# Optimization experiments

Measured on AMD Instinct MI355X. Metric: run time of the kernel, lower is better.

The kernel has to match this reference:

```python
import jax, jax.numpy as jnp
import numpy as np

H = 16          # num_heads
D_NOPE = 128    # qk_nope_head_dim
D_ROPE = 64     # qk_rope_head_dim
D_QK = 192      # qk_head_dim
D_V = 128       # v_head_dim
THETA = 10000.0
EPS = 1e-6


def rmsnorm(x, w):
    x32 = x.astype(jnp.float32)
    x32 = x32 * jax.lax.rsqrt(jnp.mean(x32 * x32, axis=-1, keepdims=True) + EPS)
    return (x32 * w).astype(x.dtype)


def rope_cos_sin(seq_len, dim, dtype):
    inv_freq = 1.0 / (THETA ** (jnp.arange(0, dim, 2, dtype=jnp.float32) / dim))  # [dim/2]
    t = jnp.arange(seq_len, dtype=jnp.float32)
    freqs = jnp.outer(t, inv_freq)  # [T, dim/2]
    return jnp.cos(freqs).astype(dtype), jnp.sin(freqs).astype(dtype)


def apply_rope(x, cos, sin):
    # x: [B, T, h, D_ROPE]; GPT-NeoX style half-split rotation
    d2 = x.shape[-1] // 2
    x1, x2 = x[..., :d2], x[..., d2:]
    c = cos[None, :, None, :]
    s = sin[None, :, None, :]
    return jnp.concatenate([x1 * c - x2 * s, x2 * c + x1 * s], axis=-1)


def setup_inputs() -> dict:
    key = jax.random.key(0)
    ks = jax.random.split(key, 8)
    B, T, D = 2, 2048, 2048
    q_lora, kv_lora = 1536, 512
    def w(k, fan_in, fan_out):
        return jax.random.normal(k, (fan_in, fan_out), dtype=jnp.float32) * (1.0 / np.sqrt(fan_in))
    return {
        "hidden_states": jax.random.normal(ks[0], (B, T, D), dtype=jnp.float32),
        "Wq_a": w(ks[1], D, q_lora),
        "q_norm_w": jnp.ones((q_lora,), dtype=jnp.float32),
        "Wq_b": w(ks[2], q_lora, H * D_QK),
        "Wk_rope": w(ks[3], D, D_ROPE),
        "Wkv_a": w(ks[4], D, kv_lora),
        "kv_norm_w": jnp.ones((kv_lora,), dtype=jnp.float32),
        "Wkv_b": w(ks[5], kv_lora, H * (D_NOPE + D_V)),
        "Wo": w(ks[6], H * D_V, D),
    }


def reference(hidden_states, Wq_a, q_norm_w, Wq_b, Wk_rope, Wkv_a, kv_norm_w, Wkv_b, Wo):
    B, T, D = hidden_states.shape
    # Q: LoRA down -> RMSNorm -> up, split into nope/rope parts
    q = rmsnorm(hidden_states @ Wq_a, q_norm_w) @ Wq_b          # [B,T,H*D_QK]
    q = q.reshape(B, T, H, D_QK)
    q_pass, q_rot = q[..., :D_NOPE], q[..., D_NOPE:]
    # KV: LoRA down -> RMSNorm -> up, split into k_nope / v
    kv = rmsnorm(hidden_states @ Wkv_a, kv_norm_w) @ Wkv_b      # [B,T,H*(D_NOPE+D_V)]
    kv = kv.reshape(B, T, H, D_NOPE + D_V)
    k_pass, v = kv[..., :D_NOPE], kv[..., D_NOPE:]
    # decoupled rope key (shared across heads)
    k_rot = (hidden_states @ Wk_rope)[:, :, None, :]            # [B,T,1,D_ROPE]
    cos, sin = rope_cos_sin(T, D_ROPE, hidden_states.dtype)
    q_rot = apply_rope(q_rot, cos, sin)
    k_rot = apply_rope(k_rot, cos, sin)
    k_rot = jnp.broadcast_to(k_rot, (B, T, H, D_ROPE))
    qf = jnp.concatenate([q_pass, q_rot], axis=-1)              # [B,T,H,D_QK]
    kf = jnp.concatenate([k_pass, k_rot], axis=-1)              # [B,T,H,D_QK]
    # causal attention, flash_attn default scale = D_QK ** -0.5
    scale = 1.0 / np.sqrt(D_QK)
    scores = jnp.einsum("bqhd,bkhd->bhqk", qf, kf) * scale
    mask = jnp.tril(jnp.ones((T, T), dtype=bool))
    scores = jnp.where(mask[None, None], scores, jnp.finfo(scores.dtype).min)
    p = jax.nn.softmax(scores, axis=-1)
    o = jnp.einsum("bhqk,bkhd->bqhd", p, v)                     # [B,T,H,D_V]
    o = o.reshape(B, T, H * D_V) @ Wo
    return o
```

## Files before the change

### kernel.cpp

```cpp
#include <hip/hip_runtime.h>
#include <cstdint>
#include <cstddef>

typedef unsigned short u16;
typedef __bf16 bf16x8 __attribute__((ext_vector_type(8)));
typedef float f32x4 __attribute__((ext_vector_type(4)));
typedef short short8 __attribute__((ext_vector_type(8)));

#define DEVI static __device__ __forceinline__

DEVI u16 f2bf(float f) {
    unsigned u = __builtin_bit_cast(unsigned, f);
    u += 0x7fffu + ((u >> 16) & 1u);
    return (u16)(u >> 16);
}
DEVI float bf2f(u16 h) {
    unsigned u = ((unsigned)h) << 16;
    return __builtin_bit_cast(float, u);
}

namespace cfg {
constexpr int B = 2, T = 2048, BT = 4096, D = 2048, QL = 1536, KVL = 512, H = 16;
constexpr int DQK = 192, DROPE = 64, DV = 128, HD = H * DQK, KVD = H * 256;
constexpr int NCAT = 2176;
}

__global__ void cvt_bf16_k(const float* __restrict__ in, u16* __restrict__ out, int n4) {
    for (int i = blockIdx.x * blockDim.x + threadIdx.x; i < n4; i += gridDim.x * blockDim.x) {
        float4 v = reinterpret_cast<const float4*>(in)[i];
        ushort4 o;
        o.x = f2bf(v.x); o.y = f2bf(v.y); o.z = f2bf(v.z); o.w = f2bf(v.w);
        reinterpret_cast<ushort4*>(out)[i] = o;
    }
}

__global__ void transpose_cvt_k(const float* __restrict__ in, u16* __restrict__ out, int R, int C) {
    __shared__ float tile[32][33];
    int tx = threadIdx.x & 31, ty = threadIdx.x >> 5;
    int c0 = blockIdx.x * 32, r0 = blockIdx.y * 32;
#pragma unroll
    for (int j = 0; j < 4; ++j)
        tile[ty + j * 8][tx] = in[(size_t)(r0 + ty + j * 8) * C + c0 + tx];
    __syncthreads();
#pragma unroll
    for (int j = 0; j < 4; ++j)
        out[(size_t)(c0 + ty + j * 8) * R + r0 + tx] = f2bf(tile[tx][ty + j * 8]);
}

__global__ void rmsnorm_k(const u16* __restrict__ x, const float* __restrict__ w,
                          u16* __restrict__ y, int C, int xs) {
    int row = blockIdx.x, tid = threadIdx.x;
    const u16* xr = x + (size_t)row * xs;
    u16* yr = y + (size_t)row * C;
    float ss = 0.f;
    for (int i = tid; i < C; i += 256) { float v = bf2f(xr[i]); ss += v * v; }
#pragma unroll
    for (int m = 32; m >= 1; m >>= 1) ss += __shfl_xor(ss, m);
    __shared__ float red[4];
    if ((tid & 63) == 0) red[tid >> 6] = ss;
    __syncthreads();
    float tot = red[0] + red[1] + red[2] + red[3];
    float rs = rsqrtf(tot / C + 1e-6f);
    for (int i = tid; i < C; i += 256) yr[i] = f2bf(bf2f(xr[i]) * rs * w[i]);
}

__global__ void rope_tab_k(float* __restrict__ ct, float* __restrict__ st) {
    int idx = blockIdx.x * 256 + threadIdx.x;
    int t = idx >> 5, i = idx & 31;
    float inv = powf(10000.f, -(float)i / 32.f);
    float f = (float)t * inv;
    ct[idx] = cosf(f);
    st[idx] = sinf(f);
}

__global__ void rope_apply_k(u16* __restrict__ x, const float* __restrict__ ct,
                             const float* __restrict__ st, int nrows, int rstride,
                             int roff, int rows_per_t) {
    int idx = blockIdx.x * 256 + threadIdx.x;
    if (idx >= nrows * 32) return;
    int row = idx >> 5, i = idx & 31;
    int t = (row / rows_per_t) % cfg::T;
    u16* p = x + (size_t)row * rstride + roff;
    float x1 = bf2f(p[i]), x2 = bf2f(p[32 + i]);
    float c = ct[t * 32 + i], s = st[t * 32 + i];
    p[i] = f2bf(x1 * c - x2 * s);
    p[32 + i] = f2bf(x2 * c + x1 * s);
}

__global__ __launch_bounds__(256) void vtrans_k(const u16* __restrict__ kv,
                                                u16* __restrict__ vt) {
    using namespace cfg;
    __shared__ u16 tl[64][136];
    const int bh = blockIdx.x, t0 = blockIdx.y * 64;
    const int b = bh >> 4, h = bh & 15;
    const int tid = threadIdx.x;
#pragma unroll
    for (int it = 0; it < 4; ++it) {
        int id = tid + it * 256, r = id >> 4, c8 = id & 15;
        short8 v = *reinterpret_cast<const short8*>(
            kv + ((size_t)(b * T + t0 + r) * H + h) * 256 + 128 + c8 * 8);
        *reinterpret_cast<short8*>(&tl[r][c8 * 8]) = v;
    }
    __syncthreads();
#pragma unroll
    for (int it = 0; it < 4; ++it) {
        int id = tid + it * 256, d = id >> 3, tc = id & 7;
        short8 v;
#pragma unroll
        for (int j = 0; j < 8; ++j) v[j] = (short)tl[tc * 8 + j][d];
        *reinterpret_cast<short8*>(vt + ((size_t)bh * 128 + d) * T + t0 + tc * 8) = v;
    }
}

template <int BM, int BN, int BK, int WM, int WN, bool OUTF32>
__global__ __launch_bounds__((BM / WM) * (BN / WN) * 64) void gemm_bt_k(
    const u16* __restrict__ A, const u16* __restrict__ Bt, void* __restrict__ Cv,
    int M, int N, int K, float cscale) {
    constexpr int NW = (BM / WM) * (BN / WN);
    constexpr int MFR = WM / 16, NFR = WN / 16;
    constexpr int NWN = BN / WN;
    __shared__ u16 As[BM * BK];
    __shared__ u16 Bs[BN * BK];
    const int tid = threadIdx.x, lane = tid & 63, wid = tid >> 6;
    const int wr = wid / NWN, wc = wid % NWN;
    const int tM = blockIdx.x * BM, tN = blockIdx.y * BN;
    const int lr = lane & 15, hi = lane >> 4;
    f32x4 acc[MFR][NFR] = {};
    for (int k0 = 0; k0 < K; k0 += BK) {
        constexpr int ACH = BM * BK * 2 / NW;
#pragma unroll
        for (int c = 0; c < ACH / 1024; ++c) {
            int loff = wid * ACH + c * 1024;
            int eidx = (loff >> 1) + lane * 8;
            const u16* src = A + (size_t)(tM + eidx / BK) * K + k0 + (eidx % BK);
            __builtin_amdgcn_global_load_lds(
                (const __attribute__((address_space(1))) void*)src,
                (__attribute__((address_space(3))) void*)((char*)As + loff), 16, 0, 0);
        }
        constexpr int BCH = BN * BK * 2 / NW;
#pragma unroll
        for (int c = 0; c < BCH / 1024; ++c) {
            int loff = wid * BCH + c * 1024;
            int eidx = (loff >> 1) + lane * 8;
            const u16* src = Bt + (size_t)(tN + eidx / BK) * K + k0 + (eidx % BK);
            __builtin_amdgcn_global_load_lds(
                (const __attribute__((address_space(1))) void*)src,
                (__attribute__((address_space(3))) void*)((char*)Bs + loff), 16, 0, 0);
        }
        __syncthreads();
#pragma unroll
        for (int kk = 0; kk < BK / 32; ++kk) {
            bf16x8 af[MFR], bfv[NFR];
#pragma unroll
            for (int mi = 0; mi < MFR; ++mi)
                af[mi] = *reinterpret_cast<const bf16x8*>(&As[(wr * WM + mi * 16 + lr) * BK + kk * 32 + hi * 8]);
#pragma unroll
            for (int ni = 0; ni < NFR; ++ni)
                bfv[ni] = *reinterpret_cast<const bf16x8*>(&Bs[(wc * WN + ni * 16 + lr) * BK + kk * 32 + hi * 8]);
#pragma unroll
            for (int mi = 0; mi < MFR; ++mi)
#pragma unroll
                for (int ni = 0; ni < NFR; ++ni)
                    acc[mi][ni] = __builtin_amdgcn_mfma_f32_16x16x32_bf16(af[mi], bfv[ni], acc[mi][ni], 0, 0, 0);
        }
        __syncthreads();
    }
#pragma unroll
    for (int mi = 0; mi < MFR; ++mi)
#pragma unroll
        for (int ni = 0; ni < NFR; ++ni)
#pragma unroll
            for (int r = 0; r < 4; ++r) {
                int row = tM + wr * WM + mi * 16 + hi * 4 + r;
                int col = tN + wc * WN + ni * 16 + lr;
                float v = acc[mi][ni][r] * cscale;
                if (OUTF32)
                    ((float*)Cv)[(size_t)row * N + col] = v;
                else
                    ((u16*)Cv)[(size_t)row * N + col] = f2bf(v);
            }
}

namespace acfg {
constexpr int QB = 64, KB = 64, KS = 200, VTS = 72, PS = 72;
constexpr int NQT = cfg::T / QB;
}
__global__ __launch_bounds__(256) void mla_attn_k(const u16* __restrict__ q,
                                                  const u16* __restrict__ kv,
                                                  const u16* __restrict__ kr, int krs,
                                                  const u16* __restrict__ vtg,
                                                  u16* __restrict__ o) {
    using namespace cfg;
    using namespace acfg;
    __shared__ u16 Ks[KB * KS];
    __shared__ u16 Vt[DV * VTS];
    __shared__ u16 Pl[4 * 16 * PS];
    const int bid = blockIdx.x;
    const int bh = bid & 31;
    const int qt = NQT - 1 - (bid >> 5);
    const int b = bh >> 4, h = bh & 15;
    const int q0 = qt * QB;
    const int tid = threadIdx.x, lane = tid & 63, w = tid >> 6;
    const int lr = lane & 15, hi = lane >> 4;

    bf16x8 qf[6];
    {
        int row = q0 + w * 16 + lr;
        const u16* qp = q + ((size_t)(b * T + row) * H + h) * DQK;
#pragma unroll
        for (int ks = 0; ks < 6; ++ks)
            qf[ks] = *reinterpret_cast<const bf16x8*>(qp + ks * 32 + hi * 8);
    }
    f32x4 oacc[8] = {};
    float lsum[4] = {0.f, 0.f, 0.f, 0.f};

    const int nkb = qt + 1;
#pragma unroll 1
    for (int kb = 0; kb < nkb; ++kb) {
        const int kt0 = kb * KB;
#pragma unroll
        for (int it = 0; it < 4; ++it) {
            int id = tid + it * 256, r = id >> 4, c8 = id & 15;
            short8 v = *reinterpret_cast<const short8*>(
                kv + ((size_t)(b * T + kt0 + r) * H + h) * 256 + c8 * 8);
            *reinterpret_cast<short8*>(&Ks[r * KS + c8 * 8]) = v;
        }
#pragma unroll
        for (int it = 0; it < 2; ++it) {
            int id = tid + it * 256, r = id >> 3, c8 = id & 7;
            short8 v = *reinterpret_cast<const short8*>(
                kr + (size_t)(b * T + kt0 + r) * krs + c8 * 8);
            *reinterpret_cast<short8*>(&Ks[r * KS + 128 + c8 * 8]) = v;
        }
#pragma unroll
        for (int it = 0; it < 4; ++it) {
            int id = tid + it * 256, d = id >> 3, c8 = id & 7;
            short8 v = *reinterpret_cast<const short8*>(
                vtg + ((size_t)(b * H + h) * 128 + d) * T + kt0 + c8 * 8);
            *reinterpret_cast<short8*>(&Vt[d * VTS + c8 * 8]) = v;
        }
        __syncthreads();

        f32x4 s[4] = {};
#pragma unroll
        for (int ks = 0; ks < 6; ++ks) {
            bf16x8 kf[4];
#pragma unroll
            for (int ni = 0; ni < 4; ++ni)
                kf[ni] = *reinterpret_cast<const bf16x8*>(&Ks[(ni * 16 + lr) * KS + ks * 32 + hi * 8]);
#pragma unroll
            for (int ni = 0; ni < 4; ++ni)
                s[ni] = __builtin_amdgcn_mfma_f32_16x16x32_bf16(qf[ks], kf[ni], s[ni], 0, 0, 0);
        }
        const bool diag = (kb == nkb - 1);
        if (diag) {
#pragma unroll
            for (int r = 0; r < 4; ++r) {
                int qr = q0 + w * 16 + hi * 4 + r;
#pragma unroll
                for (int ni = 0; ni < 4; ++ni) {
                    int kc = kt0 + ni * 16 + lr;
                    if (kc > qr) s[ni][r] = -INFINITY;
                }
            }
        }
        u16* pw = &Pl[w * 16 * PS];
#pragma unroll
        for (int r = 0; r < 4; ++r) {
            float p0 = exp2f(s[0][r]);
            float p1 = exp2f(s[1][r]);
            float p2 = exp2f(s[2][r]);
            float p3 = exp2f(s[3][r]);
            lsum[r] += (p0 + p1) + (p2 + p3);
            pw[(hi * 4 + r) * PS + 0 * 16 + lr] = __builtin_bit_cast(u16, (__bf16)p0);
            pw[(hi * 4 + r) * PS + 1 * 16 + lr] = __builtin_bit_cast(u16, (__bf16)p1);
            pw[(hi * 4 + r) * PS + 2 * 16 + lr] = __builtin_bit_cast(u16, (__bf16)p2);
            pw[(hi * 4 + r) * PS + 3 * 16 + lr] = __builtin_bit_cast(u16, (__bf16)p3);
        }
#pragma unroll
        for (int kk = 0; kk < 2; ++kk) {
            bf16x8 pf = *reinterpret_cast<const bf16x8*>(&pw[lr * PS + kk * 32 + hi * 8]);
#pragma unroll
            for (int ni = 0; ni < 8; ++ni) {
                bf16x8 vf = *reinterpret_cast<const bf16x8*>(&Vt[(ni * 16 + lr) * VTS + kk * 32 + hi * 8]);
                oacc[ni] = __builtin_amdgcn_mfma_f32_16x16x32_bf16(pf, vf, oacc[ni], 0, 0, 0);
            }
        }
        __syncthreads();
    }
    float ltot[4];
#pragma unroll
    for (int r = 0; r < 4; ++r) {
        float sumv = lsum[r];
        sumv += __shfl_xor(sumv, 1);
        sumv += __shfl_xor(sumv, 2);
        sumv += __shfl_xor(sumv, 4);
        sumv += __shfl_xor(sumv, 8);
        ltot[r] = 1.f / sumv;
    }
#pragma unroll
    for (int ni = 0; ni < 8; ++ni)
#pragma unroll
        for (int r = 0; r < 4; ++r) {
            int row = q0 + w * 16 + hi * 4 + r;
            int col = ni * 16 + lr;
            float v = oacc[ni][r] * ltot[r];
            o[((size_t)(b * T + row) * H + h) * DV + col] = f2bf(v);
        }
}

namespace wso {
using namespace cfg;
constexpr size_t O_HSVT = 0;
constexpr size_t O_WCAT = O_HSVT + (size_t)BT * D * 2;
constexpr size_t O_WQB  = O_WCAT + (size_t)NCAT * D * 2;
constexpr size_t O_WKVB = O_WQB  + (size_t)HD * QL * 2;
constexpr size_t O_WO   = O_WKVB + (size_t)KVD * KVL * 2;
constexpr size_t O_QAKR = O_WO   + (size_t)D * D * 2;
constexpr size_t O_QAN  = O_QAKR + (size_t)BT * NCAT * 2;
constexpr size_t O_KVAN = O_QAN;
constexpr size_t O_QB   = O_QAN  + (size_t)BT * QL * 2;
constexpr size_t O_KV   = O_QB   + (size_t)BT * HD * 2;
constexpr size_t O_COS  = O_KV   + (size_t)BT * KVD * 2;
constexpr size_t O_SIN  = O_COS  + (size_t)T * 32 * 4;
constexpr size_t O_OB   = O_SIN  + (size_t)T * 32 * 4;
}

extern "C" void kernel_launch(void* const* d_in, const int* in_sizes, int n_in,
                              void* d_out, int out_size, void* d_ws, size_t ws_size,
                              hipStream_t stream) {
    using namespace cfg;
    using namespace wso;
    (void)in_sizes; (void)n_in; (void)out_size; (void)ws_size;

    const float* hs   = (const float*)d_in[0];
    const float* Wqa  = (const float*)d_in[1];
    const float* qnw  = (const float*)d_in[2];
    const float* Wqb  = (const float*)d_in[3];
    const float* Wkr  = (const float*)d_in[4];
    const float* Wkva = (const float*)d_in[5];
    const float* kvnw = (const float*)d_in[6];
    const float* Wkvb = (const float*)d_in[7];
    const float* Wo   = (const float*)d_in[8];

    char* ws = (char*)d_ws;
    u16* hs_b   = (u16*)(ws + O_HSVT);
    u16* vtg    = (u16*)(ws + O_HSVT);
    u16* wcat   = (u16*)(ws + O_WCAT);
    u16* wqb_t  = (u16*)(ws + O_WQB);
    u16* wkvb_t = (u16*)(ws + O_WKVB);
    u16* wo_t   = (u16*)(ws + O_WO);
    u16* qakr   = (u16*)(ws + O_QAKR);
    u16* qan    = (u16*)(ws + O_QAN);
    u16* kvan   = (u16*)(ws + O_KVAN);
    u16* qb     = (u16*)(ws + O_QB);
    u16* kvb    = (u16*)(ws + O_KV);
    float* cost = (float*)(ws + O_COS);
    float* sint = (float*)(ws + O_SIN);
    u16* ob     = (u16*)(ws + O_OB);

    const float qesc = 0.07216878364870323f * 1.4426950408889634f;

    cvt_bf16_k<<<2048, 256, 0, stream>>>(hs, hs_b, BT * D / 4);
    transpose_cvt_k<<<dim3(QL / 32, D / 32), 256, 0, stream>>>(Wqa, wcat, D, QL);
    transpose_cvt_k<<<dim3(KVL / 32, D / 32), 256, 0, stream>>>(Wkva, wcat + (size_t)QL * D, D, KVL);
    transpose_cvt_k<<<dim3(DROPE / 32, D / 32), 256, 0, stream>>>(Wkr, wcat + (size_t)(QL + KVL) * D, D, DROPE);
    transpose_cvt_k<<<dim3(HD / 32, QL / 32), 256, 0, stream>>>(Wqb, wqb_t, QL, HD);
    transpose_cvt_k<<<dim3(KVD / 32, KVL / 32), 256, 0, stream>>>(Wkvb, wkvb_t, KVL, KVD);
    transpose_cvt_k<<<dim3(D / 32, D / 32), 256, 0, stream>>>(Wo, wo_t, D, D);
    rope_tab_k<<<T * 32 / 256, 256, 0, stream>>>(cost, sint);
    gemm_bt_k<128, 128, 32, 64, 64, false><<<dim3(BT / 128, NCAT / 128), 256, 0, stream>>>(
        hs_b, wcat, qakr, BT, NCAT, D, 1.f);
    rmsnorm_k<<<BT, 256, 0, stream>>>(qakr, qnw, qan, QL, NCAT);
    gemm_bt_k<128, 128, 32, 64, 64, false><<<dim3(BT / 128, HD / 128), 256, 0, stream>>>(
        qan, wqb_t, qb, BT, HD, QL, qesc);
    rope_apply_k<<<BT * H * 32 / 256, 256, 0, stream>>>(qb, cost, sint, BT * H, DQK, 128, H);
    rmsnorm_k<<<BT, 256, 0, stream>>>(qakr + QL, kvnw, kvan, KVL, NCAT);
    gemm_bt_k<128, 128, 32, 64, 64, false><<<dim3(BT / 128, KVD / 128), 256, 0, stream>>>(
        kvan, wkvb_t, kvb, BT, KVD, KVL, 1.f);
    rope_apply_k<<<BT * 32 / 256, 256, 0, stream>>>(qakr + QL + KVL, cost, sint, BT, NCAT, 0, 1);
    vtrans_k<<<dim3(B * H, T / 64), 256, 0, stream>>>(kvb, vtg);
    mla_attn_k<<<32 * acfg::NQT, 256, 0, stream>>>(qb, kvb, qakr + QL + KVL, NCAT, vtg, ob);
    gemm_bt_k<128, 128, 32, 64, 64, true><<<dim3(BT / 128, D / 128), 256, 0, stream>>>(
        ob, wo_t, d_out, BT, D, H * DV, 1.f);
}
```

Baseline: 541.9 us.

## Double-buffer GEMM LDS tiles and prefetch attention K/V tiles into registers

```diff
diff --git a/kernel.cpp b/kernel.cpp
--- a/kernel.cpp
+++ b/kernel.cpp
@@ -119,14 +119,15 @@
     constexpr int NW = (BM / WM) * (BN / WN);
     constexpr int MFR = WM / 16, NFR = WN / 16;
     constexpr int NWN = BN / WN;
-    __shared__ u16 As[BM * BK];
-    __shared__ u16 Bs[BN * BK];
+    __shared__ u16 As[2][BM * BK];
+    __shared__ u16 Bs[2][BN * BK];
     const int tid = threadIdx.x, lane = tid & 63, wid = tid >> 6;
     const int wr = wid / NWN, wc = wid % NWN;
     const int tM = blockIdx.x * BM, tN = blockIdx.y * BN;
     const int lr = lane & 15, hi = lane >> 4;
     f32x4 acc[MFR][NFR] = {};
-    for (int k0 = 0; k0 < K; k0 += BK) {
+
+    auto STAGE = [&](int k0, int buf) {
         constexpr int ACH = BM * BK * 2 / NW;
 #pragma unroll
         for (int c = 0; c < ACH / 1024; ++c) {
@@ -135,7 +136,7 @@
             const u16* src = A + (size_t)(tM + eidx / BK) * K + k0 + (eidx % BK);
             __builtin_amdgcn_global_load_lds(
                 (const __attribute__((address_space(1))) void*)src,
-                (__attribute__((address_space(3))) void*)((char*)As + loff), 16, 0, 0);
+                (__attribute__((address_space(3))) void*)((char*)As[buf] + loff), 16, 0, 0);
         }
         constexpr int BCH = BN * BK * 2 / NW;
 #pragma unroll
@@ -145,18 +146,24 @@
             const u16* src = Bt + (size_t)(tN + eidx / BK) * K + k0 + (eidx % BK);
             __builtin_amdgcn_global_load_lds(
                 (const __attribute__((address_space(1))) void*)src,
-                (__attribute__((address_space(3))) void*)((char*)Bs + loff), 16, 0, 0);
-        }
-        __syncthreads();
+                (__attribute__((address_space(3))) void*)((char*)Bs[buf] + loff), 16, 0, 0);
+        }
+    };
+
+    STAGE(0, 0);
+    __syncthreads();
+    int cur = 0;
+    for (int k0 = 0; k0 < K; k0 += BK) {
+        if (k0 + BK < K) STAGE(k0 + BK, cur ^ 1);
 #pragma unroll
         for (int kk = 0; kk < BK / 32; ++kk) {
             bf16x8 af[MFR], bfv[NFR];
 #pragma unroll
             for (int mi = 0; mi < MFR; ++mi)
-                af[mi] = *reinterpret_cast<const bf16x8*>(&As[(wr * WM + mi * 16 + lr) * BK + kk * 32 + hi * 8]);
+                af[mi] = *reinterpret_cast<const bf16x8*>(&As[cur][(wr * WM + mi * 16 + lr) * BK + kk * 32 + hi * 8]);
 #pragma unroll
             for (int ni = 0; ni < NFR; ++ni)
-                bfv[ni] = *reinterpret_cast<const bf16x8*>(&Bs[(wc * WN + ni * 16 + lr) * BK + kk * 32 + hi * 8]);
+                bfv[ni] = *reinterpret_cast<const bf16x8*>(&Bs[cur][(wc * WN + ni * 16 + lr) * BK + kk * 32 + hi * 8]);
 #pragma unroll
             for (int mi = 0; mi < MFR; ++mi)
 #pragma unroll
@@ -164,6 +171,7 @@
                     acc[mi][ni] = __builtin_amdgcn_mfma_f32_16x16x32_bf16(af[mi], bfv[ni], acc[mi][ni], 0, 0, 0);
         }
         __syncthreads();
+        cur ^= 1;
     }
 #pragma unroll
     for (int mi = 0; mi < MFR; ++mi)
@@ -214,32 +222,56 @@
     f32x4 oacc[8] = {};
     float lsum[4] = {0.f, 0.f, 0.f, 0.f};
 
+    short8 rkn[4], rkr[2], rv[4];
+    auto LOADT = [&](int kb) {
+        const int kt0 = kb * KB;
+#pragma unroll
+        for (int it = 0; it < 4; ++it) {
+            int id = tid + it * 256, r = id >> 4, c8 = id & 15;
+            rkn[it] = *reinterpret_cast<const short8*>(
+                kv + ((size_t)(b * T + kt0 + r) * H + h) * 256 + c8 * 8);
+        }
+#pragma unroll
+        for (int it = 0; it < 2; ++it) {
+            int id = tid + it * 256, r = id >> 3, c8 = id & 7;
+            rkr[it] = *reinterpret_cast<const short8*>(
+                kr + (size_t)(b * T + kt0 + r) * krs + c8 * 8);
+        }
+#pragma unroll
+        for (int it = 0; it < 4; ++it) {
+            int id = tid + it * 256, d = id >> 3, c8 = id & 7;
+            rv[it] = *reinterpret_cast<const short8*>(
+                vtg + ((size_t)(b * H + h) * 128 + d) * T + kt0 + c8 * 8);
+        }
+    };
+    auto WRITET = [&]() {
+#pragma unroll
+        for (int it = 0; it < 4; ++it) {
+            int id = tid + it * 256, r = id >> 4, c8 = id & 15;
+            *reinterpret_cast<short8*>(&Ks[r * KS + c8 * 8]) = rkn[it];
+        }
+#pragma unroll
+        for (int it = 0; it < 2; ++it) {
+            int id = tid + it * 256, r = id >> 3, c8 = id & 7;
+            *reinterpret_cast<short8*>(&Ks[r * KS + 128 + c8 * 8]) = rkr[it];
+        }
+#pragma unroll
+        for (int it = 0; it < 4; ++it) {
+            int id = tid + it * 256, d = id >> 3, c8 = id & 7;
+            *reinterpret_cast<short8*>(&Vt[d * VTS + c8 * 8]) = rv[it];
+        }
+    };
+
     const int nkb = qt + 1;
+    LOADT(0);
+    WRITET();
+    __syncthreads();
+
 #pragma unroll 1
     for (int kb = 0; kb < nkb; ++kb) {
         const int kt0 = kb * KB;
-#pragma unroll
-        for (int it = 0; it < 4; ++it) {
-            int id = tid + it * 256, r = id >> 4, c8 = id & 15;
-            short8 v = *reinterpret_cast<const short8*>(
-                kv + ((size_t)(b * T + kt0 + r) * H + h) * 256 + c8 * 8);
-            *reinterpret_cast<short8*>(&Ks[r * KS + c8 * 8]) = v;
-        }
-#pragma unroll
-        for (int it = 0; it < 2; ++it) {
-            int id = tid + it * 256, r = id >> 3, c8 = id & 7;
-            short8 v = *reinterpret_cast<const short8*>(
-                kr + (size_t)(b * T + kt0 + r) * krs + c8 * 8);
-            *reinterpret_cast<short8*>(&Ks[r * KS + 128 + c8 * 8]) = v;
-        }
-#pragma unroll
-        for (int it = 0; it < 4; ++it) {
-            int id = tid + it * 256, d = id >> 3, c8 = id & 7;
-            short8 v = *reinterpret_cast<const short8*>(
-                vtg + ((size_t)(b * H + h) * 128 + d) * T + kt0 + c8 * 8);
-            *reinterpret_cast<short8*>(&Vt[d * VTS + c8 * 8]) = v;
-        }
-        __syncthreads();
+        const bool more = (kb + 1 < nkb);
+        if (more) LOADT(kb + 1);
 
         f32x4 s[4] = {};
 #pragma unroll
@@ -287,6 +319,10 @@
             }
         }
         __syncthreads();
+        if (more) {
+            WRITET();
+            __syncthreads();
+        }
     }
     float ltot[4];
 #pragma unroll
```

Measured after the change: 448.7 us. 1.21x faster.
